# Optimization experiments

Measured on AMD Instinct MI355X. Metric: run time of the kernel, lower is better.

The kernel has to match this reference:

```python
import jax, jax.numpy as jnp
import numpy as np

N_NODES = 50000
N_EDGES = 800000
IN_DIM = 100
OUT_DIM = 40
K_HOPS = 3


def setup_inputs() -> dict:
    key = jax.random.key(0)
    k1, k2, k3, k4 = jax.random.split(key, 4)
    feat = jax.random.normal(k1, (N_NODES, IN_DIM), dtype=jnp.float32)
    # fc params (PyTorch Linear default init scale ~ 1/sqrt(in_dim))
    W = jax.random.normal(k2, (OUT_DIM, IN_DIM), dtype=jnp.float32) / np.sqrt(IN_DIM)
    b = jnp.zeros((OUT_DIM,), dtype=jnp.float32)
    src = jax.random.randint(k3, (N_EDGES,), 0, N_NODES, dtype=jnp.int32)
    dst = jax.random.randint(k4, (N_EDGES,), 0, N_NODES, dtype=jnp.int32)
    return {"feat": feat, "W": W, "b": b, "src": src, "dst": dst}


def reference(feat, W, b, src, dst):
    n = feat.shape[0]
    # symmetric degree norm (DGL SGConv uses in-degrees, clamp(min=1))
    deg = jax.ops.segment_sum(jnp.ones_like(dst, dtype=feat.dtype), dst, num_segments=n)
    norm = jnp.maximum(deg, 1.0)[:, None] ** -0.5  # [N,1]
    h = feat
    for _ in range(K_HOPS):
        h = h * norm
        # SpMM: sum over incoming edges (gather src rows, scatter-add to dst)
        h = jax.ops.segment_sum(h[src], dst, num_segments=n)
        h = h * norm
    # user-supplied normalize: per-feature zero mean / unit std (unbiased std)
    h = (h - h.mean(axis=0)) / h.std(axis=0, ddof=1)
    # final linear classifier
    return h @ W.T + b
```

## Files before the change

### kernel.cpp

```cpp
#include <hip/hip_runtime.h>

#define N_NODES 50000
#define N_EDGES 800000
#define IN_DIM 100
#define OUT_DIM 40
#define ROW 50
#define ROW_PAD 64
#define SCAN_B 512
#define NSCAN_BLK ((N_NODES + SCAN_B - 1) / SCAN_B)
#define CSR_CAP (N_EDGES + N_NODES * 8 + 64)

typedef unsigned int uint;

__device__ __forceinline__ float bflo(uint u) { return __uint_as_float(u << 16); }
__device__ __forceinline__ float bfhi(uint u) { return __uint_as_float(u & 0xffff0000u); }
__device__ __forceinline__ uint packbf(float a, float b) {
    uint ua = __float_as_uint(a), ub = __float_as_uint(b);
    ua = (ua + 0x7fffu + ((ua >> 16) & 1u)) >> 16;
    ub = (ub + 0x7fffu + ((ub >> 16) & 1u)) >> 16;
    return ua | (ub << 16);
}

__global__ void zero_kernel(int* p, int n, uint* fs, uint* bufA, uint* bufB) {
    int i = blockIdx.x * blockDim.x + threadIdx.x;
    if (i < n) p[i] = 0;
    if (i < ROW_PAD) {
        fs[(size_t)N_NODES * ROW_PAD + i] = 0u;
        bufA[(size_t)N_NODES * ROW_PAD + i] = 0u;
        bufB[(size_t)N_NODES * ROW_PAD + i] = 0u;
    }
}

__global__ void deg_kernel(const int* __restrict__ dst, int* __restrict__ deg,
                           int* __restrict__ eoff) {
    int e = blockIdx.x * blockDim.x + threadIdx.x;
    if (e < N_EDGES) eoff[e] = atomicAdd(&deg[dst[e]], 1);
}

__global__ __launch_bounds__(SCAN_B) void scan1_kernel(const int* __restrict__ deg,
                                                       int* __restrict__ rowptr,
                                                       float* __restrict__ norm,
                                                       float* __restrict__ norm2,
                                                       int* __restrict__ blocksum) {
    int i = blockIdx.x * SCAN_B + threadIdx.x;
    int lane = threadIdx.x & 63, wid = threadIdx.x >> 6;
    int d = (i < N_NODES) ? deg[i] : 0;
    int da = (d + 7) & ~7;
    int v = da;
#pragma unroll
    for (int off = 1; off < 64; off <<= 1) {
        int t = __shfl_up(v, off);
        if (lane >= off) v += t;
    }
    __shared__ int wsum[8];
    if (lane == 63) wsum[wid] = v;
    __syncthreads();
    if (threadIdx.x < 8) {
        int w = wsum[threadIdx.x];
#pragma unroll
        for (int off = 1; off < 8; off <<= 1) {
            int t = __shfl_up(w, off);
            if (lane >= off) w += t;
        }
        wsum[threadIdx.x] = w;
    }
    __syncthreads();
    int woff = wid ? wsum[wid - 1] : 0;
    int incl = woff + v;
    if (i < N_NODES) {
        rowptr[i] = incl - da;
        float n1 = 1.0f / sqrtf((float)max(d, 1));
        norm[i] = n1;
        norm2[i] = n1 * n1;
    }
    if (threadIdx.x == SCAN_B - 1) blocksum[blockIdx.x] = incl;
}

__global__ __launch_bounds__(128) void scan2_kernel(const int* __restrict__ blocksum,
                                                    int* __restrict__ blockoff,
                                                    int* __restrict__ rowptr) {
    __shared__ int s[128];
    int t = threadIdx.x;
    int v = (t < NSCAN_BLK) ? blocksum[t] : 0;
    s[t] = v;
    __syncthreads();
    for (int off = 1; off < 128; off <<= 1) {
        int u = (t >= off) ? s[t - off] : 0;
        __syncthreads();
        s[t] += u;
        __syncthreads();
    }
    if (t < NSCAN_BLK) blockoff[t] = s[t] - v;
    if (t == 127) rowptr[N_NODES] = s[127];
}

__global__ __launch_bounds__(SCAN_B) void scan3_kernel(int* __restrict__ rowptr,
                                                       const int* __restrict__ blockoff,
                                                       const int* __restrict__ deg,
                                                       int* __restrict__ csr) {
    int i = blockIdx.x * SCAN_B + threadIdx.x;
    if (i < N_NODES) {
        int rp = rowptr[i] + blockoff[blockIdx.x];
        rowptr[i] = rp;
        int d = deg[i], da = (d + 7) & ~7;
        for (int k = d; k < da; ++k) csr[rp + k] = N_NODES;
    }
}

__global__ void csr_fill_kernel(const int* __restrict__ src, const int* __restrict__ dst,
                                const int* __restrict__ rowptr,
                                const int* __restrict__ eoff,
                                int* __restrict__ csr) {
    int e = blockIdx.x * blockDim.x + threadIdx.x;
    if (e < N_EDGES) csr[rowptr[dst[e]] + eoff[e]] = src[e];
}

__global__ __launch_bounds__(256) void prescale_kernel(const float* __restrict__ feat,
                                                       const float* __restrict__ norm,
                                                       uint4* __restrict__ fs4) {
    int t = blockIdx.x * 256 + threadIdx.x;
    if (t >= N_NODES * 16) return;
    int n = t >> 4, ql = t & 15;
    float nm = norm[n];
    uint4 o = make_uint4(0u, 0u, 0u, 0u);
    const float4* fr = (const float4*)(feat + (size_t)n * IN_DIM);
    if (ql < 12) {
        float4 a = fr[2 * ql], b2 = fr[2 * ql + 1];
        o.x = packbf(a.x * nm, a.y * nm);  o.y = packbf(a.z * nm, a.w * nm);
        o.z = packbf(b2.x * nm, b2.y * nm); o.w = packbf(b2.z * nm, b2.w * nm);
    } else if (ql == 12) {
        float4 a = fr[24];
        o.x = packbf(a.x * nm, a.y * nm);  o.y = packbf(a.z * nm, a.w * nm);
    }
    fs4[t] = o;
}

__global__ __launch_bounds__(128) void spmm_kernel(const uint4* __restrict__ H4,
                                                   const int* __restrict__ rowptr,
                                                   const int* __restrict__ csr,
                                                   const float* __restrict__ scale,
                                                   uint4* __restrict__ out4) {
    const int n = blockIdx.x * 2 + (threadIdx.x >> 6);
    const int l = threadIdx.x & 63;
    const int q = l >> 4;
    const int ql = l & 15;
    const int beg = rowptr[n], end = rowptr[n + 1];
    float ax0 = 0.f, ax1 = 0.f, ax2 = 0.f, ax3 = 0.f;
    float ay0 = 0.f, ay1 = 0.f, ay2 = 0.f, ay3 = 0.f;
    for (int j = beg; j < end; j += 8) {
        int s0 = csr[j + q];
        int s1 = csr[j + 4 + q];
        uint4 u0 = H4[(size_t)s0 * 16 + ql];
        uint4 u1 = H4[(size_t)s1 * 16 + ql];
        ax0 += bflo(u0.x); ay0 += bfhi(u0.x);
        ax1 += bflo(u0.y); ay1 += bfhi(u0.y);
        ax2 += bflo(u0.z); ay2 += bfhi(u0.z);
        ax3 += bflo(u0.w); ay3 += bfhi(u0.w);
        ax0 += bflo(u1.x); ay0 += bfhi(u1.x);
        ax1 += bflo(u1.y); ay1 += bfhi(u1.y);
        ax2 += bflo(u1.z); ay2 += bfhi(u1.z);
        ax3 += bflo(u1.w); ay3 += bfhi(u1.w);
    }
    ax0 += __shfl_xor(ax0, 16); ax1 += __shfl_xor(ax1, 16);
    ax2 += __shfl_xor(ax2, 16); ax3 += __shfl_xor(ax3, 16);
    ay0 += __shfl_xor(ay0, 16); ay1 += __shfl_xor(ay1, 16);
    ay2 += __shfl_xor(ay2, 16); ay3 += __shfl_xor(ay3, 16);
    ax0 += __shfl_xor(ax0, 32); ax1 += __shfl_xor(ax1, 32);
    ax2 += __shfl_xor(ax2, 32); ax3 += __shfl_xor(ax3, 32);
    ay0 += __shfl_xor(ay0, 32); ay1 += __shfl_xor(ay1, 32);
    ay2 += __shfl_xor(ay2, 32); ay3 += __shfl_xor(ay3, 32);
    if (q == 0) {
        float sc = scale[n];
        uint4 o;
        o.x = packbf(ax0 * sc, ay0 * sc);
        o.y = packbf(ax1 * sc, ay1 * sc);
        o.z = packbf(ax2 * sc, ay2 * sc);
        o.w = packbf(ax3 * sc, ay3 * sc);
        out4[(size_t)n * 16 + ql] = o;
    }
}

#define CS_BLOCKS 625
#define CS_THREADS 256
__global__ __launch_bounds__(CS_THREADS) void col_stats_kernel(const uint* __restrict__ h,
                                                               float* __restrict__ colsum,
                                                               float* __restrict__ colsq) {
    int gtid = blockIdx.x * CS_THREADS + threadIdx.x;
    const int stride = CS_BLOCKS * CS_THREADS;
    const int total = N_NODES * ROW_PAD;
    float s0 = 0.f, s1 = 0.f, q0 = 0.f, q1 = 0.f;
    for (int i = gtid; i < total; i += stride) {
        uint u = h[i];
        float a = bflo(u), b = bfhi(u);
        s0 += a; s1 += b; q0 += a * a; q1 += b * b;
    }
    __shared__ float ssum[IN_DIM], ssq[IN_DIM];
    if (threadIdx.x < IN_DIM) { ssum[threadIdx.x] = 0.f; ssq[threadIdx.x] = 0.f; }
    __syncthreads();
    int p = gtid & 63;
    if (p < ROW) {
        atomicAdd(&ssum[2 * p], s0);
        atomicAdd(&ssum[2 * p + 1], s1);
        atomicAdd(&ssq[2 * p], q0);
        atomicAdd(&ssq[2 * p + 1], q1);
    }
    __syncthreads();
    if (threadIdx.x < IN_DIM) {
        atomicAdd(&colsum[threadIdx.x], ssum[threadIdx.x]);
        atomicAdd(&colsq[threadIdx.x], ssq[threadIdx.x]);
    }
}

__global__ __launch_bounds__(256) void prep_kernel(const float* __restrict__ colsum,
                                                   const float* __restrict__ colsq,
                                                   const float* __restrict__ W,
                                                   const float* __restrict__ b,
                                                   float* __restrict__ Wt,
                                                   float* __restrict__ bp) {
    __shared__ float smean[IN_DIM];
    __shared__ float sinv[IN_DIM];
    int t = threadIdx.x;
    const float Nf = (float)N_NODES;
    if (t < IN_DIM) {
        float m = colsum[t] / Nf;
        float var = (colsq[t] - Nf * m * m) / (Nf - 1.0f);
        var = fmaxf(var, 1e-20f);
        smean[t] = m;
        sinv[t] = 1.0f / sqrtf(var);
    }
    __syncthreads();
    for (int i = t; i < IN_DIM * OUT_DIM; i += 256) {
        int o = i % OUT_DIM, f = i / OUT_DIM;
        Wt[f * OUT_DIM + o] = W[o * IN_DIM + f] * sinv[f];
    }
    if (t < OUT_DIM) {
        float acc = b[t];
        for (int f = 0; f < IN_DIM; ++f)
            acc -= smean[f] * W[t * IN_DIM + f] * sinv[f];
        bp[t] = acc;
    }
}

__global__ __launch_bounds__(256) void final_kernel(const uint4* __restrict__ h4,
                                                    const float* __restrict__ Wt,
                                                    const float* __restrict__ bp,
                                                    float* __restrict__ out) {
    __shared__ float sW[104 * OUT_DIM];
    __shared__ float sb[OUT_DIM];
    for (int i = threadIdx.x; i < 104 * OUT_DIM; i += 256)
        sW[i] = (i < IN_DIM * OUT_DIM) ? Wt[i] : 0.f;
    if (threadIdx.x < OUT_DIM) sb[threadIdx.x] = bp[threadIdx.x];
    __syncthreads();
    int t = blockIdx.x * 256 + threadIdx.x;
    if (t >= N_NODES * 10) return;
    int n = t / 10;
    int og = (t - n * 10) * 4;
    const uint4* hr = h4 + (size_t)n * 16;
    float a0 = sb[og], a1 = sb[og + 1], a2 = sb[og + 2], a3 = sb[og + 3];
#pragma unroll
    for (int r = 0; r < 13; ++r) {
        uint4 u = hr[r];
        int f = r * 8;
        float v0 = bflo(u.x), v1 = bfhi(u.x), v2 = bflo(u.y), v3 = bfhi(u.y);
        float v4 = bflo(u.z), v5 = bfhi(u.z), v6 = bflo(u.w), v7 = bfhi(u.w);
        const float* w0 = &sW[(f + 0) * OUT_DIM + og];
        const float* w1 = &sW[(f + 1) * OUT_DIM + og];
        const float* w2 = &sW[(f + 2) * OUT_DIM + og];
        const float* w3 = &sW[(f + 3) * OUT_DIM + og];
        const float* w4 = &sW[(f + 4) * OUT_DIM + og];
        const float* w5 = &sW[(f + 5) * OUT_DIM + og];
        const float* w6 = &sW[(f + 6) * OUT_DIM + og];
        const float* w7 = &sW[(f + 7) * OUT_DIM + og];
        a0 += v0 * w0[0] + v1 * w1[0] + v2 * w2[0] + v3 * w3[0]
            + v4 * w4[0] + v5 * w5[0] + v6 * w6[0] + v7 * w7[0];
        a1 += v0 * w0[1] + v1 * w1[1] + v2 * w2[1] + v3 * w3[1]
            + v4 * w4[1] + v5 * w5[1] + v6 * w6[1] + v7 * w7[1];
        a2 += v0 * w0[2] + v1 * w1[2] + v2 * w2[2] + v3 * w3[2]
            + v4 * w4[2] + v5 * w5[2] + v6 * w6[2] + v7 * w7[2];
        a3 += v0 * w0[3] + v1 * w1[3] + v2 * w2[3] + v3 * w3[3]
            + v4 * w4[3] + v5 * w5[3] + v6 * w6[3] + v7 * w7[3];
    }
    float4 o = make_float4(a0, a1, a2, a3);
    *((float4*)(out + (size_t)n * OUT_DIM + og)) = o;
}

extern "C" void kernel_launch(void* const* d_in, const int* in_sizes, int n_in,
                              void* d_out, int out_size, void* d_ws, size_t ws_size,
                              hipStream_t stream) {
    const float* feat = (const float*)d_in[0];
    const float* W    = (const float*)d_in[1];
    const float* b    = (const float*)d_in[2];
    const int*   src  = (const int*)d_in[3];
    const int*   dst  = (const int*)d_in[4];
    float* out = (float*)d_out;

    char* w = (char*)d_ws;
    int*   deg      = (int*)w;    w += N_NODES * 4;
    float* colsum   = (float*)w;  w += 128 * 4;
    float* colsq    = (float*)w;  w += 128 * 4;
    int*   eoff     = (int*)w;    w += N_EDGES * 4;
    int*   rowptr   = (int*)w;    w += 50004 * 4;
    float* norm     = (float*)w;  w += N_NODES * 4;
    float* norm2    = (float*)w;  w += N_NODES * 4;
    int*   blocksum = (int*)w;    w += 128 * 4;
    int*   blockoff = (int*)w;    w += 128 * 4;
    int*   csr      = (int*)w;    w += CSR_CAP * 4;
    float* Wt       = (float*)w;  w += IN_DIM * OUT_DIM * 4;
    float* bp       = (float*)w;  w += 64 * 4;
    w = (char*)(((size_t)w + 255) & ~(size_t)255);
    const size_t HB = (size_t)(N_NODES + 1) * ROW_PAD * 4;
    uint*  fs       = (uint*)w;   w += HB;
    uint*  bufA     = (uint*)w;   w += HB;
    uint*  bufB     = (uint*)w;   w += HB;

    {
        int nz = N_NODES + 256;
        zero_kernel<<<(nz + 255) / 256, 256, 0, stream>>>(deg, nz, fs, bufA, bufB);
    }
    deg_kernel<<<(N_EDGES + 255) / 256, 256, 0, stream>>>(dst, deg, eoff);
    scan1_kernel<<<NSCAN_BLK, SCAN_B, 0, stream>>>(deg, rowptr, norm, norm2, blocksum);
    scan2_kernel<<<1, 128, 0, stream>>>(blocksum, blockoff, rowptr);
    scan3_kernel<<<NSCAN_BLK, SCAN_B, 0, stream>>>(rowptr, blockoff, deg, csr);
    csr_fill_kernel<<<(N_EDGES + 255) / 256, 256, 0, stream>>>(src, dst, rowptr, eoff, csr);
    prescale_kernel<<<(N_NODES * 16 + 255) / 256, 256, 0, stream>>>(feat, norm, (uint4*)fs);
    spmm_kernel<<<N_NODES / 2, 128, 0, stream>>>((const uint4*)fs, rowptr, csr, norm2, (uint4*)bufA);
    spmm_kernel<<<N_NODES / 2, 128, 0, stream>>>((const uint4*)bufA, rowptr, csr, norm2, (uint4*)bufB);
    spmm_kernel<<<N_NODES / 2, 128, 0, stream>>>((const uint4*)bufB, rowptr, csr, norm, (uint4*)bufA);
    col_stats_kernel<<<CS_BLOCKS, CS_THREADS, 0, stream>>>(bufA, colsum, colsq);
    prep_kernel<<<1, 256, 0, stream>>>(colsum, colsq, W, b, Wt, bp);
    {
        int total = N_NODES * 10;
        final_kernel<<<(total + 255) / 256, 256, 0, stream>>>((const uint4*)bufA, Wt, bp, out);
    }
}
```

Measured before the change: 266.6 us.

## Fuse small setup kernels to cut launch count

Drops the zero kernel in favour of a memset, merges scan2 and scan3 by having each block serially sum the block totals, fuses CSR fill, prescale and pad-row zeroing into one launch, and folds the weight/bias prep into the final kernel. It also adds an unroll hint to the SpMM edge loop. The aim is to remove launch overhead and the serial single-block kernels. In exchange, every final_kernel block recomputes the normalized weights and bias redundantly, and each scan block loops over about 98 block sums serially.

```diff
diff --git a/kernel.cpp b/kernel.cpp
--- a/kernel.cpp
+++ b/kernel.cpp
@@ -19,16 +19,6 @@
     ua = (ua + 0x7fffu + ((ua >> 16) & 1u)) >> 16;
     ub = (ub + 0x7fffu + ((ub >> 16) & 1u)) >> 16;
     return ua | (ub << 16);
-}
-
-__global__ void zero_kernel(int* p, int n, uint* fs, uint* bufA, uint* bufB) {
-    int i = blockIdx.x * blockDim.x + threadIdx.x;
-    if (i < n) p[i] = 0;
-    if (i < ROW_PAD) {
-        fs[(size_t)N_NODES * ROW_PAD + i] = 0u;
-        bufA[(size_t)N_NODES * ROW_PAD + i] = 0u;
-        bufB[(size_t)N_NODES * ROW_PAD + i] = 0u;
-    }
 }
 
 __global__ void deg_kernel(const int* __restrict__ dst, int* __restrict__ deg,
@@ -76,63 +66,68 @@
     if (threadIdx.x == SCAN_B - 1) blocksum[blockIdx.x] = incl;
 }
 
-__global__ __launch_bounds__(128) void scan2_kernel(const int* __restrict__ blocksum,
-                                                    int* __restrict__ blockoff,
-                                                    int* __restrict__ rowptr) {
-    __shared__ int s[128];
-    int t = threadIdx.x;
-    int v = (t < NSCAN_BLK) ? blocksum[t] : 0;
-    s[t] = v;
-    __syncthreads();
-    for (int off = 1; off < 128; off <<= 1) {
-        int u = (t >= off) ? s[t - off] : 0;
-        __syncthreads();
-        s[t] += u;
-        __syncthreads();
-    }
-    if (t < NSCAN_BLK) blockoff[t] = s[t] - v;
-    if (t == 127) rowptr[N_NODES] = s[127];
-}
-
-__global__ __launch_bounds__(SCAN_B) void scan3_kernel(int* __restrict__ rowptr,
-                                                       const int* __restrict__ blockoff,
-                                                       const int* __restrict__ deg,
-                                                       int* __restrict__ csr) {
-    int i = blockIdx.x * SCAN_B + threadIdx.x;
+__global__ __launch_bounds__(SCAN_B) void scan23_kernel(int* __restrict__ rowptr,
+                                                        const int* __restrict__ blocksum,
+                                                        const int* __restrict__ deg,
+                                                        int* __restrict__ csr) {
+    __shared__ int s_boff, s_tot;
+    int t = threadIdx.x, bb = blockIdx.x;
+    if (t == 0) {
+        int boff = 0, tot = 0;
+        for (int j = 0; j < NSCAN_BLK; ++j) {
+            int v = blocksum[j];
+            tot += v;
+            if (j < bb) boff += v;
+        }
+        s_boff = boff;
+        s_tot = tot;
+    }
+    __syncthreads();
+    int i = bb * SCAN_B + t;
     if (i < N_NODES) {
-        int rp = rowptr[i] + blockoff[blockIdx.x];
+        int rp = rowptr[i] + s_boff;
         rowptr[i] = rp;
         int d = deg[i], da = (d + 7) & ~7;
         for (int k = d; k < da; ++k) csr[rp + k] = N_NODES;
     }
-}
-
-__global__ void csr_fill_kernel(const int* __restrict__ src, const int* __restrict__ dst,
-                                const int* __restrict__ rowptr,
-                                const int* __restrict__ eoff,
-                                int* __restrict__ csr) {
-    int e = blockIdx.x * blockDim.x + threadIdx.x;
-    if (e < N_EDGES) csr[rowptr[dst[e]] + eoff[e]] = src[e];
-}
-
-__global__ __launch_bounds__(256) void prescale_kernel(const float* __restrict__ feat,
-                                                       const float* __restrict__ norm,
-                                                       uint4* __restrict__ fs4) {
-    int t = blockIdx.x * 256 + threadIdx.x;
-    if (t >= N_NODES * 16) return;
-    int n = t >> 4, ql = t & 15;
-    float nm = norm[n];
-    uint4 o = make_uint4(0u, 0u, 0u, 0u);
-    const float4* fr = (const float4*)(feat + (size_t)n * IN_DIM);
-    if (ql < 12) {
-        float4 a = fr[2 * ql], b2 = fr[2 * ql + 1];
-        o.x = packbf(a.x * nm, a.y * nm);  o.y = packbf(a.z * nm, a.w * nm);
-        o.z = packbf(b2.x * nm, b2.y * nm); o.w = packbf(b2.z * nm, b2.w * nm);
-    } else if (ql == 12) {
-        float4 a = fr[24];
-        o.x = packbf(a.x * nm, a.y * nm);  o.y = packbf(a.z * nm, a.w * nm);
-    }
-    fs4[t] = o;
+    if (bb == 0 && t == 0) rowptr[N_NODES] = s_tot;
+}
+
+__global__ __launch_bounds__(256) void fill_kernel(const int* __restrict__ src,
+                                                   const int* __restrict__ dst,
+                                                   const int* __restrict__ rowptr,
+                                                   const int* __restrict__ eoff,
+                                                   int* __restrict__ csr,
+                                                   const float* __restrict__ feat,
+                                                   const float* __restrict__ norm,
+                                                   uint4* __restrict__ fs4,
+                                                   uint4* __restrict__ bufA4,
+                                                   uint4* __restrict__ bufB4) {
+    const int T1 = N_EDGES, T2 = N_NODES * 16;
+    int task = blockIdx.x * 256 + threadIdx.x;
+    if (task < T1) {
+        csr[rowptr[dst[task]] + eoff[task]] = src[task];
+    } else if (task < T1 + T2) {
+        int qq = task - T1;
+        int n = qq >> 4, ql = qq & 15;
+        float nm = norm[n];
+        uint4 o = make_uint4(0u, 0u, 0u, 0u);
+        const float4* fr = (const float4*)(feat + (size_t)n * IN_DIM);
+        if (ql < 12) {
+            float4 a = fr[2 * ql], b2 = fr[2 * ql + 1];
+            o.x = packbf(a.x * nm, a.y * nm);  o.y = packbf(a.z * nm, a.w * nm);
+            o.z = packbf(b2.x * nm, b2.y * nm); o.w = packbf(b2.z * nm, b2.w * nm);
+        } else if (ql == 12) {
+            float4 a = fr[24];
+            o.x = packbf(a.x * nm, a.y * nm);  o.y = packbf(a.z * nm, a.w * nm);
+        }
+        fs4[qq] = o;
+    } else if (task < T1 + T2 + 48) {
+        int k = task - T1 - T2;
+        uint4 z = make_uint4(0u, 0u, 0u, 0u);
+        uint4* dp = (k < 16) ? fs4 : (k < 32) ? bufA4 : bufB4;
+        dp[(size_t)N_NODES * 16 + (k & 15)] = z;
+    }
 }
 
 __global__ __launch_bounds__(128) void spmm_kernel(const uint4* __restrict__ H4,
@@ -147,6 +142,7 @@
     const int beg = rowptr[n], end = rowptr[n + 1];
     float ax0 = 0.f, ax1 = 0.f, ax2 = 0.f, ax3 = 0.f;
     float ay0 = 0.f, ay1 = 0.f, ay2 = 0.f, ay3 = 0.f;
+#pragma unroll 2
     for (int j = beg; j < end; j += 8) {
         int s0 = csr[j + q];
         int s1 = csr[j + 4 + q];
@@ -211,45 +207,34 @@
     }
 }
 
-__global__ __launch_bounds__(256) void prep_kernel(const float* __restrict__ colsum,
-                                                   const float* __restrict__ colsq,
-                                                   const float* __restrict__ W,
-                                                   const float* __restrict__ b,
-                                                   float* __restrict__ Wt,
-                                                   float* __restrict__ bp) {
-    __shared__ float smean[IN_DIM];
-    __shared__ float sinv[IN_DIM];
-    int t = threadIdx.x;
-    const float Nf = (float)N_NODES;
-    if (t < IN_DIM) {
-        float m = colsum[t] / Nf;
-        float var = (colsq[t] - Nf * m * m) / (Nf - 1.0f);
-        var = fmaxf(var, 1e-20f);
-        smean[t] = m;
-        sinv[t] = 1.0f / sqrtf(var);
-    }
-    __syncthreads();
-    for (int i = t; i < IN_DIM * OUT_DIM; i += 256) {
-        int o = i % OUT_DIM, f = i / OUT_DIM;
-        Wt[f * OUT_DIM + o] = W[o * IN_DIM + f] * sinv[f];
-    }
-    if (t < OUT_DIM) {
-        float acc = b[t];
-        for (int f = 0; f < IN_DIM; ++f)
-            acc -= smean[f] * W[t * IN_DIM + f] * sinv[f];
-        bp[t] = acc;
-    }
-}
-
 __global__ __launch_bounds__(256) void final_kernel(const uint4* __restrict__ h4,
-                                                    const float* __restrict__ Wt,
-                                                    const float* __restrict__ bp,
+                                                    const float* __restrict__ colsum,
+                                                    const float* __restrict__ colsq,
+                                                    const float* __restrict__ W,
+                                                    const float* __restrict__ b,
                                                     float* __restrict__ out) {
     __shared__ float sW[104 * OUT_DIM];
     __shared__ float sb[OUT_DIM];
-    for (int i = threadIdx.x; i < 104 * OUT_DIM; i += 256)
-        sW[i] = (i < IN_DIM * OUT_DIM) ? Wt[i] : 0.f;
-    if (threadIdx.x < OUT_DIM) sb[threadIdx.x] = bp[threadIdx.x];
+    const float Nf = (float)N_NODES;
+    for (int i = threadIdx.x; i < 104 * OUT_DIM; i += 256) {
+        int f = i / OUT_DIM, o = i - f * OUT_DIM;
+        float wv = 0.f;
+        if (f < IN_DIM) {
+            float m = colsum[f] / Nf;
+            float var = fmaxf((colsq[f] - Nf * m * m) / (Nf - 1.0f), 1e-20f);
+            wv = W[o * IN_DIM + f] * rsqrtf(var);
+        }
+        sW[i] = wv;
+    }
+    if (threadIdx.x < OUT_DIM) {
+        float acc = b[threadIdx.x];
+        for (int f = 0; f < IN_DIM; ++f) {
+            float m = colsum[f] / Nf;
+            float var = fmaxf((colsq[f] - Nf * m * m) / (Nf - 1.0f), 1e-20f);
+            acc -= m * W[threadIdx.x * IN_DIM + f] * rsqrtf(var);
+        }
+        sb[threadIdx.x] = acc;
+    }
     __syncthreads();
     int t = blockIdx.x * 256 + threadIdx.x;
     if (t >= N_NODES * 10) return;
@@ -303,33 +288,30 @@
     float* norm     = (float*)w;  w += N_NODES * 4;
     float* norm2    = (float*)w;  w += N_NODES * 4;
     int*   blocksum = (int*)w;    w += 128 * 4;
-    int*   blockoff = (int*)w;    w += 128 * 4;
     int*   csr      = (int*)w;    w += CSR_CAP * 4;
-    float* Wt       = (float*)w;  w += IN_DIM * OUT_DIM * 4;
-    float* bp       = (float*)w;  w += 64 * 4;
     w = (char*)(((size_t)w + 255) & ~(size_t)255);
     const size_t HB = (size_t)(N_NODES + 1) * ROW_PAD * 4;
     uint*  fs       = (uint*)w;   w += HB;
     uint*  bufA     = (uint*)w;   w += HB;
     uint*  bufB     = (uint*)w;   w += HB;
 
-    {
-        int nz = N_NODES + 256;
-        zero_kernel<<<(nz + 255) / 256, 256, 0, stream>>>(deg, nz, fs, bufA, bufB);
-    }
+    hipMemsetAsync(d_ws, 0, (size_t)(N_NODES + 256) * 4, stream);
     deg_kernel<<<(N_EDGES + 255) / 256, 256, 0, stream>>>(dst, deg, eoff);
     scan1_kernel<<<NSCAN_BLK, SCAN_B, 0, stream>>>(deg, rowptr, norm, norm2, blocksum);
-    scan2_kernel<<<1, 128, 0, stream>>>(blocksum, blockoff, rowptr);
-    scan3_kernel<<<NSCAN_BLK, SCAN_B, 0, stream>>>(rowptr, blockoff, deg, csr);
-    csr_fill_kernel<<<(N_EDGES + 255) / 256, 256, 0, stream>>>(src, dst, rowptr, eoff, csr);
-    prescale_kernel<<<(N_NODES * 16 + 255) / 256, 256, 0, stream>>>(feat, norm, (uint4*)fs);
+    scan23_kernel<<<NSCAN_BLK, SCAN_B, 0, stream>>>(rowptr, blocksum, deg, csr);
+    {
+        int total = N_EDGES + N_NODES * 16 + 48;
+        fill_kernel<<<(total + 255) / 256, 256, 0, stream>>>(
+            src, dst, rowptr, eoff, csr, feat, norm,
+            (uint4*)fs, (uint4*)bufA, (uint4*)bufB);
+    }
     spmm_kernel<<<N_NODES / 2, 128, 0, stream>>>((const uint4*)fs, rowptr, csr, norm2, (uint4*)bufA);
     spmm_kernel<<<N_NODES / 2, 128, 0, stream>>>((const uint4*)bufA, rowptr, csr, norm2, (uint4*)bufB);
     spmm_kernel<<<N_NODES / 2, 128, 0, stream>>>((const uint4*)bufB, rowptr, csr, norm, (uint4*)bufA);
     col_stats_kernel<<<CS_BLOCKS, CS_THREADS, 0, stream>>>(bufA, colsum, colsq);
-    prep_kernel<<<1, 256, 0, stream>>>(colsum, colsq, W, b, Wt, bp);
     {
         int total = N_NODES * 10;
-        final_kernel<<<(total + 255) / 256, 256, 0, stream>>>((const uint4*)bufA, Wt, bp, out);
-    }
-}
+        final_kernel<<<(total + 255) / 256, 256, 0, stream>>>(
+            (const uint4*)bufA, colsum, colsq, W, b, out);
+    }
+}
```

Result: no change. 270.8 us (+1.6%).
